# Optimization experiments

Measured on AMD Instinct MI355X. Metric: run time of the kernel, lower is better.

Reference implementation:

```python
import jax, jax.numpy as jnp
import numpy as np

TOPK = 8
BN_EPS = 1e-5


def setup_inputs() -> dict:
    key = jax.random.key(0)
    ks = jax.random.split(key, 5)
    b, n, d = 2, 1024, 1024
    h, nk, kd = 8, 256, 128  # num_heads, num_keys (sqrt(65536)), key_dims
    ne = nk * nk             # 65536 experts
    scale = 0.02
    return {
        "inputs": jax.random.normal(ks[0], (b, n, d), jnp.float32),
        "gamma": jnp.ones((d,), jnp.float32),
        "beta": jnp.zeros((d,), jnp.float32),
        "w_q": jax.random.normal(ks[1], (2 * h * kd, d), jnp.float32) * scale,
        "keys": jax.random.normal(ks[2], (h, nk, 2, kd), jnp.float32) * scale,
        "key_in": jax.random.normal(ks[3], (ne, d), jnp.float32) * scale,
        "key_out": jax.random.normal(ks[4], (ne, d), jnp.float32) * scale,
    }


def reference(inputs, gamma, beta, w_q, keys, key_in, key_out):
    b, n, d = inputs.shape
    h, nk, _, kd = keys.shape
    k = TOPK

    # BatchNorm1d over flattened tokens (training-mode batch statistics)
    x = inputs.reshape(b * n, d)
    mu = jnp.mean(x, axis=0)
    var = jnp.mean(jnp.square(x - mu), axis=0)  # biased var, as torch BN
    xn = (x - mu) * jax.lax.rsqrt(var + BN_EPS) * gamma + beta

    # query projection -> (2, b, n, h, kd)
    q = (xn @ w_q.T).reshape(b, n, 2, h, kd).transpose(2, 0, 1, 3, 4)

    # similarity with product keys: (2, b, n, h, nk)
    sim = jnp.einsum("pbnhd,hkpd->pbnhk", q, keys)

    # stage 1: per-half top-k
    s, i = jax.lax.top_k(sim, k)          # (2, b, n, h, k)
    sx, sy = s[0], s[1]
    ix, iy = i[0], i[1]

    # stage 2: cartesian combine then top-k of k*k
    all_scores = (sx[..., :, None] + sy[..., None, :]).reshape(b, n, h, k * k)
    all_idx = (ix[..., :, None] * nk + iy[..., None, :]).reshape(b, n, h, k * k)
    scores, pk = jax.lax.top_k(all_scores, k)          # (b, n, h, k)
    idx = jnp.take_along_axis(all_idx, pk, axis=-1)    # (b, n, h, k)

    # gather expert vectors: (b, n, h, k, d)
    w_down = key_in[idx]
    w_up = key_out[idx]

    o = jnp.einsum("bnd,bnhkd->bnhk", inputs, w_down)
    o = jax.nn.gelu(o, approximate=False) * jax.nn.softmax(scores, axis=-1)
    return jnp.einsum("bnhk,bnhkd->bnd", o, w_up)
```

## Files before the change

kernel.cpp:

```cpp
#include <hip/hip_runtime.h>
#include <math.h>

#define TT 2048
#define DD 1024
#define HH 8
#define NKK 256
#define KDD 128
#define TK 8
#define NEE 65536

#define DELTA 2e-5f

#define WS_PS    0
#define WS_PQ    262144
#define WS_A     524288
#define WS_B2    528384
#define WS_FLAG  532480
#define WS_XNH   1048576
#define WS_XNL   5242880
#define WS_Q     9437184
#define WS_SIM   26214400
#define WS_WQH   26214400
#define WS_WQL   30408704
#define WS_IDX   59768832
#define WS_SMW   60293120

typedef short bf16x8 __attribute__((ext_vector_type(8)));
typedef float f32x4 __attribute__((ext_vector_type(4)));

__global__ __launch_bounds__(256) void bn_partial(const float* __restrict__ x,
    double* __restrict__ ps, double* __restrict__ pq)
{
    int col = blockIdx.x * 256 + threadIdx.x;
    int r0 = blockIdx.y * 64;
    double s = 0.0, q = 0.0;
    for (int r = 0; r < 64; ++r) {
        double v = (double)x[(size_t)(r0 + r) * DD + col];
        s += v; q += v * v;
    }
    ps[(size_t)blockIdx.y * DD + col] = s;
    pq[(size_t)blockIdx.y * DD + col] = q;
}

__global__ __launch_bounds__(256) void bn_final(const double* __restrict__ ps,
    const double* __restrict__ pq, const float* __restrict__ gamma,
    const float* __restrict__ beta, float* __restrict__ Aout, float* __restrict__ Bout)
{
    int col = blockIdx.x * 256 + threadIdx.x;
    double s = 0.0, q = 0.0;
    for (int g = 0; g < 32; ++g) { s += ps[(size_t)g * DD + col]; q += pq[(size_t)g * DD + col]; }
    double mu = s / 2048.0;
    double var = q / 2048.0 - mu * mu;
    double rstd = 1.0 / sqrt(var + 1e-5);
    Aout[col] = (float)((double)gamma[col] * rstd);
    Bout[col] = (float)((double)beta[col] - mu * (double)gamma[col] * rstd);
}

__device__ __forceinline__ void split_bf16(float v, unsigned short& h, unsigned short& l)
{
    __bf16 hb = (__bf16)v;
    float hf = (float)hb;
    __bf16 lb = (__bf16)(v - hf);
    h = __builtin_bit_cast(unsigned short, hb);
    l = __builtin_bit_cast(unsigned short, lb);
}

__global__ __launch_bounds__(256) void xn_kernel(const float* __restrict__ x,
    const float* __restrict__ A, const float* __restrict__ B2,
    unsigned short* __restrict__ XNh, unsigned short* __restrict__ XNl)
{
    int i = blockIdx.x * 256 + threadIdx.x;
    float4 v = ((const float4*)x)[i];
    int c = (i & 255) << 2;
    v.x = v.x * A[c + 0] + B2[c + 0];
    v.y = v.y * A[c + 1] + B2[c + 1];
    v.z = v.z * A[c + 2] + B2[c + 2];
    v.w = v.w * A[c + 3] + B2[c + 3];
    ushort4 h, l;
    split_bf16(v.x, h.x, l.x); split_bf16(v.y, h.y, l.y);
    split_bf16(v.z, h.z, l.z); split_bf16(v.w, h.w, l.w);
    ((ushort4*)XNh)[i] = h;
    ((ushort4*)XNl)[i] = l;
}

__global__ __launch_bounds__(256) void wq_convert(const float* __restrict__ wq,
    unsigned short* __restrict__ Wh, unsigned short* __restrict__ Wl)
{
    int i = blockIdx.x * 256 + threadIdx.x;
    float4 v = ((const float4*)wq)[i];
    ushort4 h, l;
    split_bf16(v.x, h.x, l.x); split_bf16(v.y, h.y, l.y);
    split_bf16(v.z, h.z, l.z); split_bf16(v.w, h.w, l.w);
    ((ushort4*)Wh)[i] = h;
    ((ushort4*)Wl)[i] = l;
}

#define LSTR 40
__global__ __launch_bounds__(256) void gemm_q_mfma(
    const unsigned short* __restrict__ Ah, const unsigned short* __restrict__ Al,
    const unsigned short* __restrict__ Bh, const unsigned short* __restrict__ Bl,
    float* __restrict__ C)
{
    __shared__ unsigned short sAh[128 * LSTR], sAl[128 * LSTR];
    __shared__ unsigned short sBh[128 * LSTR], sBl[128 * LSTR];
    int tid = threadIdx.x;
    int lane = tid & 63, w = tid >> 6;
    int wm = w >> 1, wn = w & 1;
    int m0 = blockIdx.x * 128, n0 = blockIdx.y * 128;

    f32x4 acc[4][4];
#pragma unroll
    for (int i = 0; i < 4; ++i)
#pragma unroll
        for (int j = 0; j < 4; ++j)
#pragma unroll
            for (int r = 0; r < 4; ++r) acc[i][j][r] = 0.f;

    int srow = tid >> 1;
    int kc0 = (tid & 1) << 1;
    size_t gA = ((size_t)(m0 + srow) << 10) + (kc0 << 3);
    size_t gB = ((size_t)(n0 + srow) << 10) + (kc0 << 3);
    int ls = srow * LSTR + (kc0 << 3);

    int ao[4], bo[4];
#pragma unroll
    for (int i = 0; i < 4; ++i) {
        ao[i] = (wm * 64 + i * 16 + (lane & 15)) * LSTR + ((lane >> 4) << 3);
        bo[i] = (wn * 64 + i * 16 + (lane & 15)) * LSTR + ((lane >> 4) << 3);
    }

    for (int k0 = 0; k0 < 1024; k0 += 32) {
        float4 vah0 = *(const float4*)(Ah + gA + k0);
        float4 vah1 = *(const float4*)(Ah + gA + k0 + 8);
        float4 val0 = *(const float4*)(Al + gA + k0);
        float4 val1 = *(const float4*)(Al + gA + k0 + 8);
        float4 vbh0 = *(const float4*)(Bh + gB + k0);
        float4 vbh1 = *(const float4*)(Bh + gB + k0 + 8);
        float4 vbl0 = *(const float4*)(Bl + gB + k0);
        float4 vbl1 = *(const float4*)(Bl + gB + k0 + 8);
        *(float4*)(sAh + ls) = vah0;  *(float4*)(sAh + ls + 8) = vah1;
        *(float4*)(sAl + ls) = val0;  *(float4*)(sAl + ls + 8) = val1;
        *(float4*)(sBh + ls) = vbh0;  *(float4*)(sBh + ls + 8) = vbh1;
        *(float4*)(sBl + ls) = vbl0;  *(float4*)(sBl + ls + 8) = vbl1;
        __syncthreads();

        bf16x8 fah[4], fal[4], fbh[4], fbl[4];
#pragma unroll
        for (int i = 0; i < 4; ++i) {
            fah[i] = *(const bf16x8*)(sAh + ao[i]);
            fal[i] = *(const bf16x8*)(sAl + ao[i]);
            fbh[i] = *(const bf16x8*)(sBh + bo[i]);
            fbl[i] = *(const bf16x8*)(sBl + bo[i]);
        }
#pragma unroll
        for (int i = 0; i < 4; ++i)
#pragma unroll
            for (int j = 0; j < 4; ++j) {
                acc[i][j] = __builtin_amdgcn_mfma_f32_16x16x32_bf16(fah[i], fbh[j], acc[i][j], 0, 0, 0);
                acc[i][j] = __builtin_amdgcn_mfma_f32_16x16x32_bf16(fah[i], fbl[j], acc[i][j], 0, 0, 0);
                acc[i][j] = __builtin_amdgcn_mfma_f32_16x16x32_bf16(fal[i], fbh[j], acc[i][j], 0, 0, 0);
            }
        __syncthreads();
    }

    int crow = m0 + wm * 64 + ((lane >> 4) << 2);
    int ccol = n0 + wn * 64 + (lane & 15);
#pragma unroll
    for (int i = 0; i < 4; ++i)
#pragma unroll
        for (int j = 0; j < 4; ++j)
#pragma unroll
            for (int r = 0; r < 4; ++r)
                C[(size_t)(crow + i * 16 + r) * 2048 + ccol + j * 16] = acc[i][j][r];
}

__global__ __launch_bounds__(256) void gemm_nt(
    const float* __restrict__ Abase, const float* __restrict__ Bbase,
    float* __restrict__ Cbase, int lda, int ldb, int ldc, int Kdim, int mode)
{
    const float* A = Abase; const float* B = Bbase; float* C = Cbase;
    if (mode == 1) {
        int z = blockIdx.z;
        int p = z >> 3, h = z & 7;
        A += (size_t)z * 128;
        B += (size_t)h * (NKK * 2 * KDD) + (size_t)p * KDD;
        C += (size_t)p * ((size_t)TT * HH * NKK) + (size_t)h * NKK;
    }
    __shared__ float As[16][132];
    __shared__ float Bs[16][132];
    int tid = threadIdx.x;
    int tx = tid & 15, ty = tid >> 4;
    int m0 = blockIdx.x * 128, n0 = blockIdx.y * 128;
    float acc[8][8];
#pragma unroll
    for (int i = 0; i < 8; ++i)
#pragma unroll
        for (int j = 0; j < 8; ++j) acc[i][j] = 0.f;

    for (int k0 = 0; k0 < Kdim; k0 += 16) {
#pragma unroll
        for (int it = 0; it < 2; ++it) {
            int li = tid + it * 256;
            int row = li >> 2;
            int kc = (li & 3) << 2;
            float4 va = *(const float4*)(A + (size_t)(m0 + row) * lda + k0 + kc);
            As[kc + 0][row] = va.x; As[kc + 1][row] = va.y;
            As[kc + 2][row] = va.z; As[kc + 3][row] = va.w;
            float4 vb = *(const float4*)(B + (size_t)(n0 + row) * ldb + k0 + kc);
            Bs[kc + 0][row] = vb.x; Bs[kc + 1][row] = vb.y;
            Bs[kc + 2][row] = vb.z; Bs[kc + 3][row] = vb.w;
        }
        __syncthreads();
#pragma unroll
        for (int k = 0; k < 16; ++k) {
            float a[8], b[8];
            *(float4*)&a[0] = *(const float4*)&As[k][ty * 4];
            *(float4*)&a[4] = *(const float4*)&As[k][64 + ty * 4];
            *(float4*)&b[0] = *(const float4*)&Bs[k][tx * 4];
            *(float4*)&b[4] = *(const float4*)&Bs[k][64 + tx * 4];
#pragma unroll
            for (int i = 0; i < 8; ++i)
#pragma unroll
                for (int j = 0; j < 8; ++j) acc[i][j] += a[i] * b[j];
        }
        __syncthreads();
    }
#pragma unroll
    for (int i = 0; i < 8; ++i) {
        int m = m0 + ((i < 4) ? (ty * 4 + i) : (64 + ty * 4 + (i - 4)));
        float4 c0 = make_float4(acc[i][0], acc[i][1], acc[i][2], acc[i][3]);
        float4 c1 = make_float4(acc[i][4], acc[i][5], acc[i][6], acc[i][7]);
        *(float4*)(C + (size_t)m * ldc + n0 + tx * 4) = c0;
        *(float4*)(C + (size_t)m * ldc + n0 + 64 + tx * 4) = c1;
    }
}

__device__ __forceinline__ void stage1_half(float v0, float v1, float v2, float v3,
    int lane, int mode, float& keep_v, int& keep_i, float& g7, float& g8)
{
#pragma unroll
    for (int it = 0; it < 9; ++it) {
        float bv = v0; int bj = 0;
        if (v1 > bv) { bv = v1; bj = 1; }
        if (v2 > bv) { bv = v2; bj = 2; }
        if (v3 > bv) { bv = v3; bj = 3; }
        int mi = lane + (bj << 6);
        float mv = bv;
#pragma unroll
        for (int off = 1; off < 64; off <<= 1) {
            float ov = __shfl_xor(mv, off);
            int oi = __shfl_xor(mi, off);
            if (ov > mv || (ov == mv && oi < mi)) { mv = ov; mi = oi; }
        }
        int keeper = (mode == 0) ? (lane >> 3) : (lane & 7);
        if (it < 8 && keeper == it) { keep_v = mv; keep_i = mi; }
        if (it == 7) g7 = mv;
        if (it == 8) g8 = mv;
        if (mi == lane)            v0 = -INFINITY;
        else if (mi == lane + 64)  v1 = -INFINITY;
        else if (mi == lane + 128) v2 = -INFINITY;
        else if (mi == lane + 192) v3 = -INFINITY;
    }
}

__device__ __forceinline__ float stage2_write(float vx, float vy, int vix, int viy,
    int lane, int base, int* __restrict__ IDX, float* __restrict__ SMW)
{
    float mycs = vx + vy;
    int cidx = vix * NKK + viy;
    float s2[9]; int wi2[8];
#pragma unroll
    for (int it = 0; it < 9; ++it) {
        float mv = mycs; int ml = lane;
#pragma unroll
        for (int off = 1; off < 64; off <<= 1) {
            float ov = __shfl_xor(mv, off);
            int ol = __shfl_xor(ml, off);
            if (ov > mv || (ov == mv && ol < ml)) { mv = ov; ml = ol; }
        }
        s2[it] = mv;
        if (it < 8) wi2[it] = __shfl(cidx, ml);
        if (lane == ml) mycs = -INFINITY;
    }
    float e[8]; float esum = 0.f;
#pragma unroll
    for (int it = 0; it < 8; ++it) { e[it] = expf(s2[it] - s2[0]); esum += e[it]; }
    float inv = 1.f / esum;
    if (lane == 0) {
#pragma unroll
        for (int it = 0; it < 8; ++it) { IDX[base + it] = wi2[it]; SMW[base + it] = e[it] * inv; }
    }
    return s2[7] - s2[8];
}

__global__ __launch_bounds__(256) void topk_kernel(
    const float* __restrict__ SIM, int* __restrict__ IDX, float* __restrict__ SMW,
    int* __restrict__ FLAG)
{
    int gw = blockIdx.x * 4 + (threadIdx.x >> 6);
    int lane = threadIdx.x & 63;
    int t = gw >> 3, h = gw & 7;

    float vx = 0.f, vy = 0.f; int vix = 0, viy = 0;
    float g7a, g8a, g7b, g8b;

    const float* s0 = SIM + ((size_t)t * HH + h) * NKK;
    stage1_half(s0[lane], s0[lane + 64], s0[lane + 128], s0[lane + 192],
                lane, 0, vx, vix, g7a, g8a);
    const float* s1 = SIM + (size_t)TT * HH * NKK + ((size_t)t * HH + h) * NKK;
    stage1_half(s1[lane], s1[lane + 64], s1[lane + 128], s1[lane + 192],
                lane, 1, vy, viy, g7b, g8b);

    float gap2 = stage2_write(vx, vy, vix, viy, lane, gw * TK, IDX, SMW);
    if (lane == 0) {
        FLAG[gw] = ((g7a - g8a) < DELTA) | ((g7b - g8b) < DELTA) | (gap2 < DELTA);
    }
}

__global__ __launch_bounds__(64) void fixup_kernel(
    const float* __restrict__ x, const float* __restrict__ Aw,
    const float* __restrict__ B2w, const float* __restrict__ w_q,
    const float* __restrict__ keys, const int* __restrict__ FLAG,
    int* __restrict__ IDX, float* __restrict__ SMW)
{
    int row = blockIdx.x;
    if (!FLAG[row]) return;
    int t = row >> 3, h = row & 7;
    int lane = threadIdx.x;
    __shared__ float xs[DD];
    __shared__ float qs[2][KDD];
    __shared__ float sims[2][NKK];

    for (int c = lane * 4; c < DD; c += 256) {
        float4 v = *(const float4*)(x + (size_t)t * DD + c);
        v.x = v.x * Aw[c + 0] + B2w[c + 0];
        v.y = v.y * Aw[c + 1] + B2w[c + 1];
        v.z = v.z * Aw[c + 2] + B2w[c + 2];
        v.w = v.w * Aw[c + 3] + B2w[c + 3];
        *(float4*)&xs[c] = v;
    }
    __syncthreads();

    for (int p = 0; p < 2; ++p)
        for (int j = 0; j < 2; ++j) {
            int kd = lane + j * 64;
            const float* wr = w_q + ((size_t)((p * HH + h) * KDD) + kd) * DD;
            float acc = 0.f;
            for (int d = 0; d < DD; d += 4) {
                float4 wv = *(const float4*)(wr + d);
                acc += xs[d] * wv.x + xs[d + 1] * wv.y + xs[d + 2] * wv.z + xs[d + 3] * wv.w;
            }
            qs[p][kd] = acc;
        }
    __syncthreads();

    for (int p = 0; p < 2; ++p)
        for (int j = 0; j < 4; ++j) {
            int key = lane + j * 64;
            const float* kr = keys + (((size_t)h * NKK + key) * 2 + p) * KDD;
            float acc = 0.f;
            for (int d = 0; d < KDD; d += 4) {
                float4 kv = *(const float4*)(kr + d);
                acc += qs[p][d] * kv.x + qs[p][d + 1] * kv.y + qs[p][d + 2] * kv.z + qs[p][d + 3] * kv.w;
            }
            sims[p][key] = acc;
        }
    __syncthreads();

    float vx = 0.f, vy = 0.f; int vix = 0, viy = 0;
    float d0, d1, d2, d3;
    stage1_half(sims[0][lane], sims[0][lane + 64], sims[0][lane + 128], sims[0][lane + 192],
                lane, 0, vx, vix, d0, d1);
    stage1_half(sims[1][lane], sims[1][lane + 64], sims[1][lane + 128], sims[1][lane + 192],
                lane, 1, vy, viy, d2, d3);
    stage2_write(vx, vy, vix, viy, lane, row * TK, IDX, SMW);
}

__global__ __launch_bounds__(256) void expert_kernel(
    const float* __restrict__ x, const int* __restrict__ IDX,
    const float* __restrict__ SMW, const float* __restrict__ key_in,
    const float* __restrict__ key_out, float* __restrict__ out)
{
    int t = blockIdx.x;
    int tid = threadIdx.x, lane = tid & 63, w = tid >> 6;
    __shared__ float xs[DD];
    __shared__ float part[4][DD];
    *(float4*)&xs[tid * 4] = *(const float4*)(x + (size_t)t * DD + tid * 4);
    __syncthreads();
    float4 xin[4];
#pragma unroll
    for (int r = 0; r < 4; ++r) xin[r] = *(const float4*)&xs[r * 256 + lane * 4];
    float4 acc[4];
#pragma unroll
    for (int r = 0; r < 4; ++r) acc[r] = make_float4(0.f, 0.f, 0.f, 0.f);

    for (int hh2 = 0; hh2 < 2; ++hh2) {
        int hh = w * 2 + hh2;
        for (int k = 0; k < TK; ++k) {
            int base = (t * HH + hh) * TK + k;
            int e = IDX[base];
            float wt = SMW[base];
            const float* ki = key_in + (size_t)e * DD;
            const float* ko = key_out + (size_t)e * DD;
            float4 kin[4], kout[4];
#pragma unroll
            for (int r = 0; r < 4; ++r) kin[r] = *(const float4*)(ki + r * 256 + lane * 4);
#pragma unroll
            for (int r = 0; r < 4; ++r) kout[r] = *(const float4*)(ko + r * 256 + lane * 4);
            float p = 0.f;
#pragma unroll
            for (int r = 0; r < 4; ++r)
                p += xin[r].x * kin[r].x + xin[r].y * kin[r].y
                   + xin[r].z * kin[r].z + xin[r].w * kin[r].w;
#pragma unroll
            for (int off = 1; off < 64; off <<= 1) p += __shfl_xor(p, off);
            float g = 0.5f * p * (1.f + erff(p * 0.70710678118654752440f));
            float go = g * wt;
#pragma unroll
            for (int r = 0; r < 4; ++r) {
                acc[r].x += go * kout[r].x; acc[r].y += go * kout[r].y;
                acc[r].z += go * kout[r].z; acc[r].w += go * kout[r].w;
            }
        }
    }
#pragma unroll
    for (int r = 0; r < 4; ++r) *(float4*)&part[w][r * 256 + lane * 4] = acc[r];
    __syncthreads();
    int c = tid * 4;
    float4 s0 = *(const float4*)&part[0][c];
    float4 s1 = *(const float4*)&part[1][c];
    float4 s2 = *(const float4*)&part[2][c];
    float4 s3 = *(const float4*)&part[3][c];
    float4 o;
    o.x = (s0.x + s1.x) + (s2.x + s3.x);
    o.y = (s0.y + s1.y) + (s2.y + s3.y);
    o.z = (s0.z + s1.z) + (s2.z + s3.z);
    o.w = (s0.w + s1.w) + (s2.w + s3.w);
    *(float4*)(out + (size_t)t * DD + c) = o;
}

extern "C" void kernel_launch(void* const* d_in, const int* in_sizes, int n_in,
                              void* d_out, int out_size, void* d_ws, size_t ws_size,
                              hipStream_t stream)
{
    const float* x       = (const float*)d_in[0];
    const float* gamma   = (const float*)d_in[1];
    const float* beta    = (const float*)d_in[2];
    const float* w_q     = (const float*)d_in[3];
    const float* keys    = (const float*)d_in[4];
    const float* key_in  = (const float*)d_in[5];
    const float* key_out = (const float*)d_in[6];
    float* out = (float*)d_out;
    char* ws = (char*)d_ws;

    double* ps  = (double*)(ws + WS_PS);
    double* pq  = (double*)(ws + WS_PQ);
    float*  Aw  = (float*)(ws + WS_A);
    float*  B2w = (float*)(ws + WS_B2);
    int*    FLAGw = (int*)(ws + WS_FLAG);
    unsigned short* XNh = (unsigned short*)(ws + WS_XNH);
    unsigned short* XNl = (unsigned short*)(ws + WS_XNL);
    unsigned short* WQh = (unsigned short*)(ws + WS_WQH);
    unsigned short* WQl = (unsigned short*)(ws + WS_WQL);
    float*  Q   = (float*)(ws + WS_Q);
    float*  SIMw= (float*)(ws + WS_SIM);
    int*    IDXw= (int*)(ws + WS_IDX);
    float*  SMWw= (float*)(ws + WS_SMW);

    bn_partial<<<dim3(4, 32), 256, 0, stream>>>(x, ps, pq);
    bn_final<<<4, 256, 0, stream>>>(ps, pq, gamma, beta, Aw, B2w);
    xn_kernel<<<2048, 256, 0, stream>>>(x, Aw, B2w, XNh, XNl);
    wq_convert<<<2048, 256, 0, stream>>>(w_q, WQh, WQl);
    gemm_q_mfma<<<dim3(16, 16), 256, 0, stream>>>(XNh, XNl, WQh, WQl, Q);
    gemm_nt<<<dim3(16, 2, 16), 256, 0, stream>>>(Q, keys, SIMw, 2048, 256, 2048, 128, 1);
    topk_kernel<<<4096, 256, 0, stream>>>(SIMw, IDXw, SMWw, FLAGw);
    fixup_kernel<<<16384, 64, 0, stream>>>(x, Aw, B2w, w_q, keys, FLAGw, IDXw, SMWw);
    expert_kernel<<<2048, 256, 0, stream>>>(x, IDXw, SMWw, key_in, key_out, out);
}
```

Measured before the change: 443.6 us.

## Fold product keys into query weights and compute similarities with one MFMA GEMM

```diff
diff --git a/kernel.cpp b/kernel.cpp
--- a/kernel.cpp
+++ b/kernel.cpp
@@ -9,7 +9,7 @@
 #define TK 8
 #define NEE 65536
 
-#define DELTA 2e-5f
+#define DELTA 1e-4f
 
 #define WS_PS    0
 #define WS_PQ    262144
@@ -18,10 +18,9 @@
 #define WS_FLAG  532480
 #define WS_XNH   1048576
 #define WS_XNL   5242880
-#define WS_Q     9437184
+#define WS_W2H   9437184
+#define WS_W2L   17825792
 #define WS_SIM   26214400
-#define WS_WQH   26214400
-#define WS_WQL   30408704
 #define WS_IDX   59768832
 #define WS_SMW   60293120
 
@@ -83,28 +82,52 @@
     ((ushort4*)XNl)[i] = l;
 }
 
-__global__ __launch_bounds__(256) void wq_convert(const float* __restrict__ wq,
-    unsigned short* __restrict__ Wh, unsigned short* __restrict__ Wl)
-{
-    int i = blockIdx.x * 256 + threadIdx.x;
-    float4 v = ((const float4*)wq)[i];
-    ushort4 h, l;
-    split_bf16(v.x, h.x, l.x); split_bf16(v.y, h.y, l.y);
-    split_bf16(v.z, h.z, l.z); split_bf16(v.w, h.w, l.w);
-    ((ushort4*)Wh)[i] = h;
-    ((ushort4*)Wl)[i] = l;
-}
-
-#define LSTR 40
-__global__ __launch_bounds__(256) void gemm_q_mfma(
+__global__ __launch_bounds__(256) void w2_kernel(
+    const float* __restrict__ keys, const float* __restrict__ wq,
+    unsigned short* __restrict__ W2h, unsigned short* __restrict__ W2l)
+{
+    int bid = blockIdx.x;
+    int p = bid >> 8, h = (bid >> 5) & 7, kb = bid & 31;
+    int tid = threadIdx.x;
+    __shared__ float ks_[8][128];
+    {
+        int key = tid >> 5, kd0 = (tid & 31) << 2;
+        float4 kv = *(const float4*)(keys +
+            (((size_t)(h * NKK + kb * 8 + key) * 2 + p) * KDD) + kd0);
+        *(float4*)&ks_[key][kd0] = kv;
+    }
+    __syncthreads();
+    float acc[8][4] = {};
+    int c0 = tid << 2;
+    const float* wbase = wq + ((size_t)(p * 8 + h) * KDD) * DD + c0;
+    for (int kd = 0; kd < KDD; ++kd) {
+        float4 wv = *(const float4*)(wbase + (size_t)kd * DD);
+#pragma unroll
+        for (int key = 0; key < 8; ++key) {
+            float kvv = ks_[key][kd];
+            acc[key][0] += kvv * wv.x; acc[key][1] += kvv * wv.y;
+            acc[key][2] += kvv * wv.z; acc[key][3] += kvv * wv.w;
+        }
+    }
+#pragma unroll
+    for (int key = 0; key < 8; ++key) {
+        size_t n = (size_t)p * 2048 + h * NKK + kb * 8 + key;
+        ushort4 hh, ll;
+        split_bf16(acc[key][0], hh.x, ll.x); split_bf16(acc[key][1], hh.y, ll.y);
+        split_bf16(acc[key][2], hh.z, ll.z); split_bf16(acc[key][3], hh.w, ll.w);
+        *(ushort4*)(W2h + n * DD + c0) = hh;
+        *(ushort4*)(W2l + n * DD + c0) = ll;
+    }
+}
+
+__global__ __launch_bounds__(256) void gemm_sim(
     const unsigned short* __restrict__ Ah, const unsigned short* __restrict__ Al,
     const unsigned short* __restrict__ Bh, const unsigned short* __restrict__ Bl,
     float* __restrict__ C)
 {
-    __shared__ unsigned short sAh[128 * LSTR], sAl[128 * LSTR];
-    __shared__ unsigned short sBh[128 * LSTR], sBl[128 * LSTR];
-    int tid = threadIdx.x;
-    int lane = tid & 63, w = tid >> 6;
+    __shared__ unsigned short sAh[128][64], sAl[128][64];
+    __shared__ unsigned short sBh[128][64], sBl[128][64];
+    int tid = threadIdx.x, lane = tid & 63, w = tid >> 6;
     int wm = w >> 1, wn = w & 1;
     int m0 = blockIdx.x * 128, n0 = blockIdx.y * 128;
 
@@ -116,50 +139,47 @@
 #pragma unroll
             for (int r = 0; r < 4; ++r) acc[i][j][r] = 0.f;
 
-    int srow = tid >> 1;
-    int kc0 = (tid & 1) << 1;
-    size_t gA = ((size_t)(m0 + srow) << 10) + (kc0 << 3);
-    size_t gB = ((size_t)(n0 + srow) << 10) + (kc0 << 3);
-    int ls = srow * LSTR + (kc0 << 3);
-
-    int ao[4], bo[4];
-#pragma unroll
-    for (int i = 0; i < 4; ++i) {
-        ao[i] = (wm * 64 + i * 16 + (lane & 15)) * LSTR + ((lane >> 4) << 3);
-        bo[i] = (wn * 64 + i * 16 + (lane & 15)) * LSTR + ((lane >> 4) << 3);
-    }
-
-    for (int k0 = 0; k0 < 1024; k0 += 32) {
-        float4 vah0 = *(const float4*)(Ah + gA + k0);
-        float4 vah1 = *(const float4*)(Ah + gA + k0 + 8);
-        float4 val0 = *(const float4*)(Al + gA + k0);
-        float4 val1 = *(const float4*)(Al + gA + k0 + 8);
-        float4 vbh0 = *(const float4*)(Bh + gB + k0);
-        float4 vbh1 = *(const float4*)(Bh + gB + k0 + 8);
-        float4 vbl0 = *(const float4*)(Bl + gB + k0);
-        float4 vbl1 = *(const float4*)(Bl + gB + k0 + 8);
-        *(float4*)(sAh + ls) = vah0;  *(float4*)(sAh + ls + 8) = vah1;
-        *(float4*)(sAl + ls) = val0;  *(float4*)(sAl + ls + 8) = val1;
-        *(float4*)(sBh + ls) = vbh0;  *(float4*)(sBh + ls + 8) = vbh1;
-        *(float4*)(sBl + ls) = vbl0;  *(float4*)(sBl + ls + 8) = vbl1;
+    int srow = tid >> 1, shalf = tid & 1;
+    const size_t gAoff = (size_t)(m0 + srow) * 1024 + (shalf << 5);
+    const size_t gBoff = (size_t)(n0 + srow) * 1024 + (shalf << 5);
+
+    for (int k0 = 0; k0 < 1024; k0 += 64) {
+#pragma unroll
+        for (int c = 0; c < 4; ++c) {
+            int sp = ((shalf << 2) + c) ^ (srow & 7);
+            float4 vah = *(const float4*)(Ah + gAoff + k0 + (c << 3));
+            float4 val = *(const float4*)(Al + gAoff + k0 + (c << 3));
+            float4 vbh = *(const float4*)(Bh + gBoff + k0 + (c << 3));
+            float4 vbl = *(const float4*)(Bl + gBoff + k0 + (c << 3));
+            *(float4*)&sAh[srow][sp << 3] = vah;
+            *(float4*)&sAl[srow][sp << 3] = val;
+            *(float4*)&sBh[srow][sp << 3] = vbh;
+            *(float4*)&sBl[srow][sp << 3] = vbl;
+        }
         __syncthreads();
-
-        bf16x8 fah[4], fal[4], fbh[4], fbl[4];
-#pragma unroll
-        for (int i = 0; i < 4; ++i) {
-            fah[i] = *(const bf16x8*)(sAh + ao[i]);
-            fal[i] = *(const bf16x8*)(sAl + ao[i]);
-            fbh[i] = *(const bf16x8*)(sBh + bo[i]);
-            fbl[i] = *(const bf16x8*)(sBl + bo[i]);
-        }
-#pragma unroll
-        for (int i = 0; i < 4; ++i)
-#pragma unroll
-            for (int j = 0; j < 4; ++j) {
-                acc[i][j] = __builtin_amdgcn_mfma_f32_16x16x32_bf16(fah[i], fbh[j], acc[i][j], 0, 0, 0);
-                acc[i][j] = __builtin_amdgcn_mfma_f32_16x16x32_bf16(fah[i], fbl[j], acc[i][j], 0, 0, 0);
-                acc[i][j] = __builtin_amdgcn_mfma_f32_16x16x32_bf16(fal[i], fbh[j], acc[i][j], 0, 0, 0);
+#pragma unroll
+        for (int ks = 0; ks < 2; ++ks) {
+            bf16x8 fah[4], fal[4], fbh[4], fbl[4];
+#pragma unroll
+            for (int i = 0; i < 4; ++i) {
+                int ra = wm * 64 + i * 16 + (lane & 15);
+                int sa = ((ks << 2) + (lane >> 4)) ^ (ra & 7);
+                fah[i] = *(const bf16x8*)&sAh[ra][sa << 3];
+                fal[i] = *(const bf16x8*)&sAl[ra][sa << 3];
+                int rb = wn * 64 + i * 16 + (lane & 15);
+                int sb = ((ks << 2) + (lane >> 4)) ^ (rb & 7);
+                fbh[i] = *(const bf16x8*)&sBh[rb][sb << 3];
+                fbl[i] = *(const bf16x8*)&sBl[rb][sb << 3];
             }
+#pragma unroll
+            for (int i = 0; i < 4; ++i)
+#pragma unroll
+                for (int j = 0; j < 4; ++j) {
+                    acc[i][j] = __builtin_amdgcn_mfma_f32_16x16x32_bf16(fah[i], fbh[j], acc[i][j], 0, 0, 0);
+                    acc[i][j] = __builtin_amdgcn_mfma_f32_16x16x32_bf16(fah[i], fbl[j], acc[i][j], 0, 0, 0);
+                    acc[i][j] = __builtin_amdgcn_mfma_f32_16x16x32_bf16(fal[i], fbh[j], acc[i][j], 0, 0, 0);
+                }
+        }
         __syncthreads();
     }
 
@@ -171,68 +191,7 @@
         for (int j = 0; j < 4; ++j)
 #pragma unroll
             for (int r = 0; r < 4; ++r)
-                C[(size_t)(crow + i * 16 + r) * 2048 + ccol + j * 16] = acc[i][j][r];
-}
-
-__global__ __launch_bounds__(256) void gemm_nt(
-    const float* __restrict__ Abase, const float* __restrict__ Bbase,
-    float* __restrict__ Cbase, int lda, int ldb, int ldc, int Kdim, int mode)
-{
-    const float* A = Abase; const float* B = Bbase; float* C = Cbase;
-    if (mode == 1) {
-        int z = blockIdx.z;
-        int p = z >> 3, h = z & 7;
-        A += (size_t)z * 128;
-        B += (size_t)h * (NKK * 2 * KDD) + (size_t)p * KDD;
-        C += (size_t)p * ((size_t)TT * HH * NKK) + (size_t)h * NKK;
-    }
-    __shared__ float As[16][132];
-    __shared__ float Bs[16][132];
-    int tid = threadIdx.x;
-    int tx = tid & 15, ty = tid >> 4;
-    int m0 = blockIdx.x * 128, n0 = blockIdx.y * 128;
-    float acc[8][8];
-#pragma unroll
-    for (int i = 0; i < 8; ++i)
-#pragma unroll
-        for (int j = 0; j < 8; ++j) acc[i][j] = 0.f;
-
-    for (int k0 = 0; k0 < Kdim; k0 += 16) {
-#pragma unroll
-        for (int it = 0; it < 2; ++it) {
-            int li = tid + it * 256;
-            int row = li >> 2;
-            int kc = (li & 3) << 2;
-            float4 va = *(const float4*)(A + (size_t)(m0 + row) * lda + k0 + kc);
-            As[kc + 0][row] = va.x; As[kc + 1][row] = va.y;
-            As[kc + 2][row] = va.z; As[kc + 3][row] = va.w;
-            float4 vb = *(const float4*)(B + (size_t)(n0 + row) * ldb + k0 + kc);
-            Bs[kc + 0][row] = vb.x; Bs[kc + 1][row] = vb.y;
-            Bs[kc + 2][row] = vb.z; Bs[kc + 3][row] = vb.w;
-        }
-        __syncthreads();
-#pragma unroll
-        for (int k = 0; k < 16; ++k) {
-            float a[8], b[8];
-            *(float4*)&a[0] = *(const float4*)&As[k][ty * 4];
-            *(float4*)&a[4] = *(const float4*)&As[k][64 + ty * 4];
-            *(float4*)&b[0] = *(const float4*)&Bs[k][tx * 4];
-            *(float4*)&b[4] = *(const float4*)&Bs[k][64 + tx * 4];
-#pragma unroll
-            for (int i = 0; i < 8; ++i)
-#pragma unroll
-                for (int j = 0; j < 8; ++j) acc[i][j] += a[i] * b[j];
-        }
-        __syncthreads();
-    }
-#pragma unroll
-    for (int i = 0; i < 8; ++i) {
-        int m = m0 + ((i < 4) ? (ty * 4 + i) : (64 + ty * 4 + (i - 4)));
-        float4 c0 = make_float4(acc[i][0], acc[i][1], acc[i][2], acc[i][3]);
-        float4 c1 = make_float4(acc[i][4], acc[i][5], acc[i][6], acc[i][7]);
-        *(float4*)(C + (size_t)m * ldc + n0 + tx * 4) = c0;
-        *(float4*)(C + (size_t)m * ldc + n0 + 64 + tx * 4) = c1;
-    }
+                C[(size_t)(crow + i * 16 + r) * 4096 + ccol + j * 16] = acc[i][j][r];
 }
 
 __device__ __forceinline__ void stage1_half(float v0, float v1, float v2, float v3,
@@ -304,10 +263,10 @@
     float vx = 0.f, vy = 0.f; int vix = 0, viy = 0;
     float g7a, g8a, g7b, g8b;
 
-    const float* s0 = SIM + ((size_t)t * HH + h) * NKK;
+    const float* s0 = SIM + (size_t)t * 4096 + h * NKK;
     stage1_half(s0[lane], s0[lane + 64], s0[lane + 128], s0[lane + 192],
                 lane, 0, vx, vix, g7a, g8a);
-    const float* s1 = SIM + (size_t)TT * HH * NKK + ((size_t)t * HH + h) * NKK;
+    const float* s1 = SIM + (size_t)t * 4096 + 2048 + h * NKK;
     stage1_half(s1[lane], s1[lane + 64], s1[lane + 128], s1[lane + 192],
                 lane, 1, vy, viy, g7b, g8b);
 
@@ -460,9 +419,8 @@
     int*    FLAGw = (int*)(ws + WS_FLAG);
     unsigned short* XNh = (unsigned short*)(ws + WS_XNH);
     unsigned short* XNl = (unsigned short*)(ws + WS_XNL);
-    unsigned short* WQh = (unsigned short*)(ws + WS_WQH);
-    unsigned short* WQl = (unsigned short*)(ws + WS_WQL);
-    float*  Q   = (float*)(ws + WS_Q);
+    unsigned short* W2h = (unsigned short*)(ws + WS_W2H);
+    unsigned short* W2l = (unsigned short*)(ws + WS_W2L);
     float*  SIMw= (float*)(ws + WS_SIM);
     int*    IDXw= (int*)(ws + WS_IDX);
     float*  SMWw= (float*)(ws + WS_SMW);
@@ -470,9 +428,8 @@
     bn_partial<<<dim3(4, 32), 256, 0, stream>>>(x, ps, pq);
     bn_final<<<4, 256, 0, stream>>>(ps, pq, gamma, beta, Aw, B2w);
     xn_kernel<<<2048, 256, 0, stream>>>(x, Aw, B2w, XNh, XNl);
-    wq_convert<<<2048, 256, 0, stream>>>(w_q, WQh, WQl);
-    gemm_q_mfma<<<dim3(16, 16), 256, 0, stream>>>(XNh, XNl, WQh, WQl, Q);
-    gemm_nt<<<dim3(16, 2, 16), 256, 0, stream>>>(Q, keys, SIMw, 2048, 256, 2048, 128, 1);
+    w2_kernel<<<512, 256, 0, stream>>>(keys, w_q, W2h, W2l);
+    gemm_sim<<<dim3(16, 32), 256, 0, stream>>>(XNh, XNl, W2h, W2l, SIMw);
     topk_kernel<<<4096, 256, 0, stream>>>(SIMw, IDXw, SMWw, FLAGw);
     fixup_kernel<<<16384, 64, 0, stream>>>(x, Aw, B2w, w_q, keys, FLAGw, IDXw, SMWw);
     expert_kernel<<<2048, 256, 0, stream>>>(x, IDXw, SMWw, key_in, key_out, out);
```

Measured after the change: 498.7 us. +12.4%, slower.
